# Kernel optimization log

Measured on AMD Instinct MI355X. Metric: run time of the kernel, lower is better.

Reference implementation:

```python
import jax, jax.numpy as jnp
import numpy as np

B, L, D = 4, 2048, 1024
H, DH = 16, 64
W = 128            # window_len
CS, R = 32, 1      # chunk_size, chunk_rank
CACHE = 2048
NCC = CACHE // CS * R   # compressed cache vectors (64)
NCB = L // CS * R       # compressed block vectors (64)
NC = NCC + NCB          # total compressed vectors (128)
NQ = L // CS            # query chunks (64)
T = L // W              # query tiles (16)
NEG = jnp.float32(-1e30)


def _ln(x, g, b, eps=1e-5):
    m = x.mean(-1, keepdims=True)
    v = ((x - m) ** 2).mean(-1, keepdims=True)
    return (x - m) * jax.lax.rsqrt(v + eps) * g + b


def _scores(x, Wd, bd):
    # dconv_1 + per-chunk softmax over chunk_size positions
    b = x.shape[0]; nc = x.shape[1] // CS
    s = (x @ Wd + bd).reshape(b, nc, CS, H, R)
    s = jnp.transpose(s, (0, 3, 1, 4, 2))          # b,H,nc,R,CS
    return jax.nn.softmax(s.astype(jnp.float32), axis=-1).astype(x.dtype)


def _compress(x, sc):
    b = x.shape[0]; nc = x.shape[1] // CS
    xv = jnp.transpose(x.reshape(b, nc, CS, H, DH), (0, 3, 1, 2, 4))  # b,H,nc,CS,DH
    return (sc @ xv).reshape(b, H, nc * R, DH)


def _heads(x):
    b, l, _ = x.shape
    return jnp.transpose(x.reshape(b, l, H, DH), (0, 2, 1, 3))


def _rel_shift(x):
    # Transformer-XL style relative shift, chunk variant (zeros enter from padding)
    b = x.shape[0]; nc = x.shape[-1]
    x5 = jnp.transpose(x.reshape(b, H, NQ, CS, nc), (0, 1, 3, 2, 4))  # b,H,CS,NQ,nc
    xp = jnp.pad(x5, ((0, 0), (0, 0), (0, 0), (0, 0), (0, R))).reshape(b, H, CS, NQ * (nc + R))
    idx = NQ * R + jnp.arange(NQ)[:, None] * nc + jnp.arange(nc)[None, :]
    out = jnp.take(xp, idx.reshape(-1), axis=-1).reshape(b, H, CS, NQ, nc)
    return jnp.transpose(out, (0, 1, 3, 2, 4)).reshape(b, H, L, nc)


def _forward(h, h_cache, key_pe, pos_win, Wq, Wk, Wv, Wo, Wd, bd, Wr, br, Wrc, brc,
             r_r_bias, r_w_bias, g_dproj, b_dproj, g_win, b_win, mask):
    b = h.shape[0]
    q = _heads(h @ Wq) / np.float32(np.sqrt(DH))       # b,H,L,DH (pre-scaled)

    # --- compressed cache keys/values ---
    hcc = _compress(h_cache, _scores(h_cache, Wd, bd))           # b,H,NCC,DH
    hcm = jnp.transpose(hcc, (0, 2, 1, 3)).reshape(b, -1, D)
    k_cache = _heads(_ln(hcm @ Wk, g_dproj, b_dproj))
    v_cache = _heads(_ln(hcm @ Wv, g_dproj, b_dproj))

    # --- sliding window keys/values (last W of cache + current block) ---
    k_bp = h @ Wk
    v_bp = h @ Wv
    hw = h_cache[:, -W:]
    k_win = _ln(jnp.concatenate([hw @ Wk, k_bp], 1), g_win, b_win)   # b, W+L, D
    v_win = _ln(jnp.concatenate([hw @ Wv, v_bp], 1), g_win, b_win)

    # --- compressed current-block keys/values ---
    sc = _scores(h, Wd, bd)
    k_bpc = _heads(_ln(jnp.transpose(_compress(k_bp, sc), (0, 2, 1, 3)).reshape(b, -1, D), g_dproj, b_dproj))
    v_bpc = _heads(_ln(jnp.transpose(_compress(v_bp, sc), (0, 2, 1, 3)).reshape(b, -1, D), g_dproj, b_dproj))
    k_comp = jnp.concatenate([k_cache, k_bpc], 2)     # b,H,NC,DH
    v_comp = jnp.concatenate([v_cache, v_bpc], 2)

    # --- windowed attention (tiled, as_strided equivalent via gather) ---
    ti = jnp.arange(T)[:, None] * W + jnp.arange(2 * W)[None, :]     # (T, 2W)
    k_t = jnp.transpose(k_win[:, ti].reshape(b, T, 2 * W, H, DH), (0, 3, 1, 2, 4))  # b,H,T,2W,DH
    v_t = jnp.transpose(v_win[:, ti].reshape(b, T, 2 * W, H, DH), (0, 3, 1, 2, 4))
    q_t = q.reshape(b, H, T, W, DH)
    aw = jnp.einsum('bhtqd,bhtkd->bhtqk', q_t + r_w_bias, k_t)       # b,H,T,W,2W
    # diagonal extraction: row q keeps cols q+1 .. q+W (the W causal window keys)
    dcol = jnp.arange(W)[:, None] + 1 + jnp.arange(W)[None, :]       # (W, W)
    aw = jnp.take_along_axis(aw, dcol[None, None, None], axis=-1).reshape(b, H, L, W)
    pos_t = (pos_win @ Wr + br).reshape(W, H, DH)
    aw = aw + jnp.einsum('bhld,whd->bhlw', q + r_r_bias, pos_t)

    # --- compressed (chunk) attention ---
    ac = jnp.einsum('bhld,bhcd->bhlc', q, k_comp)
    pos_c = (key_pe @ Wrc + brc).reshape(NC, H, DH)
    ac = ac + _rel_shift(jnp.einsum('bhld,chd->bhlc', q, pos_c))
    ac = jnp.where(mask, NEG, ac.reshape(b, H, NQ, CS, NC)).reshape(b, H, L, NC)

    # --- joint softmax over [compressed | window] ---
    full = jax.nn.softmax(jnp.concatenate([ac, aw], -1).astype(jnp.float32), -1).astype(h.dtype)
    ac, aw = full[..., :NC], full[..., NC:]

    # --- put_tiles: scatter window probs back to tiled 2W layout (inverse of diag extract) ---
    awt = aw.reshape(b, H, T, W, W)
    awp = jnp.pad(awt, ((0, 0), (0, 0), (0, 0), (0, 0), (1, W)))     # last dim 1+2W, zeros outside band
    col = jnp.clip(jnp.arange(2 * W)[None, :] - jnp.arange(W)[:, None], 0, 2 * W)
    aw_t = jnp.take_along_axis(awp, col[None, None, None], axis=-1)  # b,H,T,W,2W

    out = jnp.einsum('bhlc,bhcd->bhld', ac, v_comp) + \
          jnp.einsum('bhtqk,bhtkd->bhtqd', aw_t, v_t).reshape(b, H, L, DH)
    out = jnp.transpose(out, (0, 2, 1, 3)).reshape(b, L, D)
    return out @ Wo


def setup_inputs() -> dict:
    key = jax.random.key(0)
    ks = jax.random.split(key, 16)
    p = lambda i, shape: jax.random.normal(ks[i], shape, jnp.float32) * 0.02
    inp = dict(
        h=jax.random.normal(ks[0], (B, L, D), jnp.float32),
        h_cache=jax.random.normal(ks[1], (B, CACHE, D), jnp.float32),
        key_pe=jax.random.normal(ks[2], (NC, D), jnp.float32),
        pos_embed_window=jax.random.normal(ks[3], (W, D), jnp.float32),
        Wq=p(4, (D, D)), Wk=p(5, (D, D)), Wv=p(6, (D, D)), Wo=p(7, (D, D)),
        Wd=p(8, (D, H * R)), bd=jnp.zeros((H * R,), jnp.float32),
        Wr=p(9, (D, D)), br=jnp.zeros((D,), jnp.float32),
        Wrc=p(10, (D, D)), brc=jnp.zeros((D,), jnp.float32),
        r_r_bias=p(11, (1, H, 1, DH)), r_w_bias=p(12, (1, H, 1, 1, DH)),
        g_dproj=jnp.ones((D,), jnp.float32), b_dproj=jnp.zeros((D,), jnp.float32),
        g_win=jnp.ones((D,), jnp.float32), b_win=jnp.zeros((D,), jnp.float32),
    )
    # causal mask over compressed vectors: bp chunk c visible to query chunk j only if c < j
    jq = jnp.arange(NQ)[:, None]
    cc = jnp.arange(NCB // R)[None, :]
    mbp = jnp.repeat(cc >= jq, R, axis=1)                         # (NQ, NCB)
    mask = jnp.concatenate([jnp.zeros((NQ, NCC), bool), mbp], axis=1)
    inp['chunked_attn_mask'] = mask[None, None, :, None, :]       # (1,1,NQ,1,NC)
    return inp


def reference(h, h_cache, key_pe, pos_embed_window, Wq, Wk, Wv, Wo, Wd, bd, Wr, br,
              Wrc, brc, r_r_bias, r_w_bias, g_dproj, b_dproj, g_win, b_win,
              chunked_attn_mask):
    return _forward(h, h_cache, key_pe, pos_embed_window, Wq, Wk, Wv, Wo, Wd, bd,
                    Wr, br, Wrc, brc, r_r_bias, r_w_bias, g_dproj, b_dproj,
                    g_win, b_win, chunked_attn_mask)
```

## Files before the change

kernel.cpp:

```cpp
#include <hip/hip_runtime.h>


typedef unsigned short u16;
typedef __attribute__((ext_vector_type(8))) short short8;
typedef __attribute__((ext_vector_type(4))) float f32x4;

#define NEGINF -1e30f

__device__ __forceinline__ float bf2f(u16 u) {
    union { unsigned int i; float f; } v; v.i = ((unsigned int)u) << 16; return v.f;
}
__device__ __forceinline__ u16 f2bf(float f) {
    union { float fl; unsigned int i; } v; v.fl = f;
    unsigned int x = v.i;
    return (u16)((x + 0x7fffu + ((x >> 16) & 1u)) >> 16);
}
__device__ __forceinline__ short8 ldg8(const u16* p) { return *(const short8*)p; }

__device__ __forceinline__ void async16(const u16* g, u16* l) {
    __builtin_amdgcn_global_load_lds(
        (const __attribute__((address_space(1))) unsigned int*)g,
        (__attribute__((address_space(3))) unsigned int*)l, 16, 0, 0);
}

__global__ __launch_bounds__(256) void cast_all(
    const float* __restrict__ h, const float* __restrict__ hc,
    const float* __restrict__ pos_w, const float* __restrict__ key_pe,
    const float* __restrict__ Wd,
    u16* __restrict__ hB, u16* __restrict__ hcwB,
    u16* __restrict__ pwB, u16* __restrict__ kpeB, u16* __restrict__ WdB)
{
    const int bx = blockIdx.x, tid = threadIdx.x;
    if (bx < 8192) {
        int i = bx * 256 + tid;
        float4 v = ((const float4*)h)[i];
        u16* o = hB + (long)i * 4;
        o[0] = f2bf(v.x); o[1] = f2bf(v.y); o[2] = f2bf(v.z); o[3] = f2bf(v.w);
    } else if (bx < 8704) {
        int i = (bx - 8192) * 256 + tid;
        int flat = i * 4;
        int b = flat >> 17, r = (flat >> 10) & 127, c = flat & 1023;
        float4 v = *(const float4*)(hc + ((long)b * 2048 + 1920 + r) * 1024 + c);
        u16* o = hcwB + (long)flat;
        o[0] = f2bf(v.x); o[1] = f2bf(v.y); o[2] = f2bf(v.z); o[3] = f2bf(v.w);
    } else if (bx < 8832) {
        int i = (bx - 8704) * 256 + tid;
        float4 v = ((const float4*)pos_w)[i];
        u16* o = pwB + (long)i * 4;
        o[0] = f2bf(v.x); o[1] = f2bf(v.y); o[2] = f2bf(v.z); o[3] = f2bf(v.w);
    } else if (bx < 8960) {
        int i = (bx - 8832) * 256 + tid;
        float4 v = ((const float4*)key_pe)[i];
        u16* o = kpeB + (long)i * 4;
        o[0] = f2bf(v.x); o[1] = f2bf(v.y); o[2] = f2bf(v.z); o[3] = f2bf(v.w);
    } else {
        int e = (bx - 8960) * 256 + tid;
        if (e < 16384) WdB[(e & 15) * 1024 + (e >> 4)] = f2bf(Wd[e]);
    }
}

__global__ __launch_bounds__(256) void cast_transpose6(
    const float* __restrict__ W0, const float* __restrict__ W1,
    const float* __restrict__ W2, const float* __restrict__ W3,
    const float* __restrict__ W4, const float* __restrict__ W5,
    u16* __restrict__ D0, u16* __restrict__ D1, u16* __restrict__ D2,
    u16* __restrict__ D3, u16* __restrict__ D4, u16* __restrict__ D5)
{
    const int z = blockIdx.z;
    const float* W = (z == 0) ? W0 : (z == 1) ? W1 : (z == 2) ? W2
                   : (z == 3) ? W3 : (z == 4) ? W4 : W5;
    u16* WT = (z == 0) ? D0 : (z == 1) ? D1 : (z == 2) ? D2
            : (z == 3) ? D3 : (z == 4) ? D4 : D5;

    __shared__ float t[32][33];
    const int bx = blockIdx.x, by = blockIdx.y;
    const int tx = threadIdx.x & 31, ty = threadIdx.x >> 5;
    #pragma unroll
    for (int p = 0; p < 4; ++p) {
        int k = by * 32 + ty + p * 8;
        t[ty + p * 8][tx] = W[(long)k * 1024 + bx * 32 + tx];
    }
    __syncthreads();
    #pragma unroll
    for (int p = 0; p < 4; ++p) {
        int n = ty + p * 8;
        WT[((long)(bx * 32 + n)) * 1024 + by * 32 + tx] = f2bf(t[tx][n]);
    }
}

#define GEMM_P3_BODY(EPILOGUE)                                                  \
    const int tid = threadIdx.x;                                                \
    const int bm = blockIdx.x, bn = blockIdx.y;                                 \
    const int K = 1024, NT = 32;                                                \
    __shared__ __align__(16) u16 As[3 * 128 * 32];                              \
    __shared__ __align__(16) u16 Bs[3 * 128 * 32];                              \
    const int lane = tid & 63, wv = tid >> 6;                                   \
    const int l15 = lane & 15, quad = lane >> 4;                                \
    const int wm = (wv & 1) * 64, wn = (wv >> 1) * 64;                          \
    f32x4 acc[4][4];                                                            \
    _Pragma("unroll")                                                           \
    for (int i = 0; i < 4; ++i)                                                 \
        _Pragma("unroll")                                                       \
        for (int j = 0; j < 4; ++j) acc[i][j] = (f32x4){0.f, 0.f, 0.f, 0.f};    \
    const int srow = wv * 32 + (lane >> 2);                                     \
    const int scol = (lane & 3) * 8;                                            \
    const u16* a_src  = A  + (long)(bm * 128 + srow) * K + scol;                \
    const u16* a_src2 = a_src + (long)16 * K;                                   \
    const u16* b_src  = Bt + (long)(bn * 128 + srow) * K + scol;                \
    const u16* b_src2 = b_src + (long)16 * K;                                   \
    const int lofs0 = (wv * 32) * 32;                                           \
    const int lofs1 = (wv * 32 + 16) * 32;                                      \
    auto stage = [&](int t, int cur) {                                          \
        const int k0 = t * 32;                                                  \
        async16(a_src  + k0, &As[cur * 4096 + lofs0]);                          \
        async16(a_src2 + k0, &As[cur * 4096 + lofs1]);                          \
        async16(b_src  + k0, &Bs[cur * 4096 + lofs0]);                          \
        async16(b_src2 + k0, &Bs[cur * 4096 + lofs1]);                          \
    };                                                                          \
    stage(0, 0); stage(1, 1);                                                   \
    int cur = 0;                                                                \
    for (int t = 0; t < NT; ++t) {                                              \
        if (t == NT - 1)                                                        \
            asm volatile("s_waitcnt vmcnt(0) lgkmcnt(0)\ns_barrier" ::: "memory"); \
        else                                                                    \
            asm volatile("s_waitcnt vmcnt(4) lgkmcnt(0)\ns_barrier" ::: "memory"); \
        int nxt = cur + 2; if (nxt >= 3) nxt -= 3;                              \
        if (t + 2 < NT) stage(t + 2, nxt);                                      \
        const u16* as = &As[cur * 4096];                                        \
        const u16* bs = &Bs[cur * 4096];                                        \
        short8 af[4], bfr[4];                                                   \
        _Pragma("unroll")                                                       \
        for (int i = 0; i < 4; ++i)                                             \
            af[i] = *(const short8*)&as[(wm + i * 16 + l15) * 32 + quad * 8];   \
        _Pragma("unroll")                                                       \
        for (int j = 0; j < 4; ++j)                                             \
            bfr[j] = *(const short8*)&bs[(wn + j * 16 + l15) * 32 + quad * 8];  \
        _Pragma("unroll")                                                       \
        for (int i = 0; i < 4; ++i)                                             \
            _Pragma("unroll")                                                   \
            for (int j = 0; j < 4; ++j)                                         \
                acc[i][j] = __builtin_amdgcn_mfma_f32_16x16x32_bf16(af[i], bfr[j], acc[i][j], 0, 0, 0); \
        cur = (cur + 1 == 3) ? 0 : cur + 1;                                     \
    }                                                                           \
    EPILOGUE

__global__ __launch_bounds__(256) void gemm_qkv3(
    const u16* __restrict__ A, const u16* __restrict__ Bt,
    u16* __restrict__ q_ws, u16* __restrict__ kbp, u16* __restrict__ vbp)
{
    GEMM_P3_BODY({
        const int mat = bn >> 3;
        _Pragma("unroll")
        for (int i = 0; i < 4; ++i) {
            _Pragma("unroll")
            for (int j = 0; j < 4; ++j) {
                int col = (bn & 7) * 128 + wn + j * 16 + l15;
                _Pragma("unroll")
                for (int r = 0; r < 4; ++r) {
                    int row = bm * 128 + wm + i * 16 + quad * 4 + r;
                    float v = acc[i][j][r];
                    long idx = (long)row * 1024 + col;
                    if (mat == 0)      q_ws[idx] = f2bf(v * 0.125f);
                    else if (mat == 1) kbp[idx] = f2bf(v);
                    else               vbp[idx] = f2bf(v);
                }
            }
        }
    })
}

__global__ __launch_bounds__(256) void gemm_out3(
    const u16* __restrict__ A, const u16* __restrict__ Bt,
    float* __restrict__ Cf)
{
    GEMM_P3_BODY({
        _Pragma("unroll")
        for (int i = 0; i < 4; ++i) {
            _Pragma("unroll")
            for (int j = 0; j < 4; ++j) {
                int col = bn * 128 + wn + j * 16 + l15;
                _Pragma("unroll")
                for (int r = 0; r < 4; ++r) {
                    int row = bm * 128 + wm + i * 16 + quad * 4 + r;
                    Cf[(long)row * 1024 + col] = acc[i][j][r];
                }
            }
        }
    })
}

struct GJob {
    const u16* A; long ab;
    const u16* Bt;
    float* Cf; u16* Cb; long cb;
    const float* bias; float scale;
};

__device__ __forceinline__ void gemm_core128(
    const GJob& j, int bz, int bm, int bn, int N, int K)
{
    const int tid = threadIdx.x;
    const u16* A = j.A + (long)bz * j.ab;
    const long coff = (long)bz * j.cb;

    __shared__ __align__(16) u16 As[128 * 32];
    __shared__ __align__(16) u16 Bs[128 * 32];

    const int lane = tid & 63, wv = tid >> 6;
    const int l15 = lane & 15, quad = lane >> 4;
    const int wm = (wv & 1) * 64, wn = (wv >> 1) * 64;

    f32x4 acc[4][4];
    #pragma unroll
    for (int i = 0; i < 4; ++i)
        #pragma unroll
        for (int jx = 0; jx < 4; ++jx) acc[i][jx] = (f32x4){0.f, 0.f, 0.f, 0.f};

    const int srow = wv * 32 + (lane >> 2);
    const int scol = (lane & 3) * 8;
    const u16* a_src  = A    + (long)(bm * 128 + srow) * K + scol;
    const u16* a_src2 = a_src + (long)16 * K;
    const u16* b_src  = j.Bt + (long)(bn * 128 + srow) * K + scol;
    const u16* b_src2 = b_src + (long)16 * K;
    u16* lA0 = &As[(wv * 32) * 32];
    u16* lA1 = &As[(wv * 32 + 16) * 32];
    u16* lB0 = &Bs[(wv * 32) * 32];
    u16* lB1 = &Bs[(wv * 32 + 16) * 32];

    for (int k0 = 0; k0 < K; k0 += 32) {
        async16(a_src, lA0); async16(a_src2, lA1);
        async16(b_src, lB0); async16(b_src2, lB1);
        a_src += 32; a_src2 += 32; b_src += 32; b_src2 += 32;
        __syncthreads();
        short8 af[4], bfr[4];
        #pragma unroll
        for (int i = 0; i < 4; ++i)
            af[i] = *(const short8*)&As[(wm + i * 16 + l15) * 32 + quad * 8];
        #pragma unroll
        for (int jx = 0; jx < 4; ++jx)
            bfr[jx] = *(const short8*)&Bs[(wn + jx * 16 + l15) * 32 + quad * 8];
        #pragma unroll
        for (int i = 0; i < 4; ++i)
            #pragma unroll
            for (int jx = 0; jx < 4; ++jx)
                acc[i][jx] = __builtin_amdgcn_mfma_f32_16x16x32_bf16(af[i], bfr[jx], acc[i][jx], 0, 0, 0);
        __syncthreads();
    }

    #pragma unroll
    for (int i = 0; i < 4; ++i) {
        #pragma unroll
        for (int jx = 0; jx < 4; ++jx) {
            int col = bn * 128 + wn + jx * 16 + l15;
            float bsv = j.bias ? j.bias[col] : 0.f;
            #pragma unroll
            for (int r = 0; r < 4; ++r) {
                int row = bm * 128 + wm + i * 16 + quad * 4 + r;
                float v = acc[i][jx][r] * j.scale + bsv;
                long idx = coff + (long)row * N + col;
                if (j.Cf) j.Cf[idx] = v;
                if (j.Cb) j.Cb[idx] = f2bf(v);
            }
        }
    }
}

__global__ __launch_bounds__(256) void gemm_dual(GJob j0, GJob j1, int nz0, int N, int K)
{
    const bool first = ((int)blockIdx.z < nz0);
    const int bz = first ? blockIdx.z : blockIdx.z - nz0;
    if (first) gemm_core128(j0, bz, blockIdx.x, blockIdx.y, N, K);
    else       gemm_core128(j1, bz, blockIdx.x, blockIdx.y, N, K);
}

__global__ __launch_bounds__(256) void gemm_multi4(GJob j0, GJob j1, GJob j2, GJob j3,
                                                   int n0, int n1, int n2, int N, int K)
{
    const int z = blockIdx.z;
    if (z < n0)                gemm_core128(j0, z, blockIdx.x, blockIdx.y, N, K);
    else if (z < n0 + n1)      gemm_core128(j1, z - n0, blockIdx.x, blockIdx.y, N, K);
    else if (z < n0 + n1 + n2) gemm_core128(j2, z - n0 - n1, blockIdx.x, blockIdx.y, N, K);
    else                       gemm_core128(j3, z - n0 - n1 - n2, blockIdx.x, blockIdx.y, N, K);
}

__global__ __launch_bounds__(256) void scores_compress2(
    const float* __restrict__ hc, const u16* __restrict__ hBp,
    const u16* __restrict__ WdB, const float* __restrict__ bd,
    u16* __restrict__ hcm, float* __restrict__ sc_blk)
{
    const int c = blockIdx.x, b = blockIdx.y;
    const bool zc = (blockIdx.z == 0);
    const int tid = threadIdx.x;
    const int lane = tid & 63, wv = tid >> 6;
    const int l15 = lane & 15, quad = lane >> 4;

    __shared__ __align__(16) u16 srcs[32][1032];
    __shared__ float sred[4][32][16];
    __shared__ float s_sm[32][16];

    if (zc) {
        const float* sb = hc + (long)b * 2048 * 1024 + (long)c * 32 * 1024;
        for (int e = tid; e < 8192; e += 256) {
            int flat = e * 4;
            int row = flat >> 10, col = flat & 1023;
            float4 v = *(const float4*)(sb + (long)row * 1024 + col);
            u16* dp = &srcs[row][col];
            dp[0] = f2bf(v.x); dp[1] = f2bf(v.y); dp[2] = f2bf(v.z); dp[3] = f2bf(v.w);
        }
    } else {
        const u16* sb = hBp + (long)b * 2048 * 1024 + (long)c * 32 * 1024;
        for (int e = tid; e < 4096; e += 256) {
            int flat = e * 8;
            int row = flat >> 10, col = flat & 1023;
            *(short8*)&srcs[row][col] = ldg8(sb + (long)row * 1024 + col);
        }
    }
    __syncthreads();

    {
        f32x4 acc0 = {0.f,0.f,0.f,0.f}, acc1 = {0.f,0.f,0.f,0.f};
        const int kq = wv * 256;
        #pragma unroll
        for (int kc = 0; kc < 8; ++kc) {
            int off = kq + kc * 32 + quad * 8;
            short8 bf_ = ldg8(WdB + (long)l15 * 1024 + off);
            short8 a0 = *(const short8*)&srcs[l15][off];
            short8 a1 = *(const short8*)&srcs[16 + l15][off];
            acc0 = __builtin_amdgcn_mfma_f32_16x16x32_bf16(a0, bf_, acc0, 0, 0, 0);
            acc1 = __builtin_amdgcn_mfma_f32_16x16x32_bf16(a1, bf_, acc1, 0, 0, 0);
        }
        #pragma unroll
        for (int r = 0; r < 4; ++r) {
            sred[wv][quad * 4 + r][l15]      = acc0[r];
            sred[wv][16 + quad * 4 + r][l15] = acc1[r];
        }
    }
    __syncthreads();
    for (int idx = tid; idx < 512; idx += 256) {
        int i = idx >> 4, hd = idx & 15;
        s_sm[i][hd] = bd[hd] + sred[0][i][hd] + sred[1][i][hd]
                            + sred[2][i][hd] + sred[3][i][hd];
    }
    __syncthreads();

    if (tid < 16) {
        int hd = tid;
        float m = NEGINF;
        for (int i = 0; i < 32; ++i) m = fmaxf(m, s_sm[i][hd]);
        float s = 0.f;
        for (int i = 0; i < 32; ++i) s += __expf(s_sm[i][hd] - m);
        float inv = 1.f / s;
        for (int i = 0; i < 32; ++i) s_sm[i][hd] = __expf(s_sm[i][hd] - m) * inv;
    }
    __syncthreads();

    if (!zc) {
        for (int idx = tid; idx < 512; idx += 256) {
            int hd = idx >> 5, i = idx & 31;
            sc_blk[(long)b * (16*64*32) + ((long)hd * 64 + c) * 32 + i] = s_sm[i][hd];
        }
    } else {
        #pragma unroll
        for (int p = 0; p < 4; ++p) {
            int j = tid + p * 256;
            int hd = j >> 6;
            float acc = 0.f;
            for (int i = 0; i < 32; ++i) acc += s_sm[i][hd] * bf2f(srcs[i][j]);
            hcm[(long)b * (64*1024) + (long)c * 1024 + j] = f2bf(acc);
        }
    }
}

__global__ __launch_bounds__(256) void compress_kv_ln(
    const u16* __restrict__ kbp, const u16* __restrict__ vbp,
    const float* __restrict__ sc,
    const float* __restrict__ g, const float* __restrict__ be,
    u16* __restrict__ k_comp, u16* __restrict__ vcT)
{
    const int c = blockIdx.x, b = blockIdx.y;
    const int tid = threadIdx.x;
    const int lane = tid & 63, wv = tid >> 6;

    __shared__ float scw[16][32];
    __shared__ float red[4][4];

    for (int idx = tid; idx < 512; idx += 256) {
        int hd = idx >> 5, i = idx & 31;
        scw[hd][i] = sc[((long)(b * 16 + hd) * 64 + c) * 32 + i];
    }
    __syncthreads();

    const int j0 = tid * 4;
    const int hd = j0 >> 6;
    float xk[4] = {0.f,0.f,0.f,0.f}, xv[4] = {0.f,0.f,0.f,0.f};
    const u16* kb = kbp + ((long)b * 2048 + c * 32) * 1024 + j0;
    const u16* vb = vbp + ((long)b * 2048 + c * 32) * 1024 + j0;
    for (int i = 0; i < 32; ++i) {
        float w = scw[hd][i];
        uint2 kr = *(const uint2*)(kb + (long)i * 1024);
        uint2 vr = *(const uint2*)(vb + (long)i * 1024);
        const u16* kp = (const u16*)&kr;
        const u16* vp = (const u16*)&vr;
        #pragma unroll
        for (int p = 0; p < 4; ++p) {
            xk[p] += w * bf2f(kp[p]);
            xv[p] += w * bf2f(vp[p]);
        }
    }
    float sk = 0.f, qk = 0.f, sv = 0.f, qv = 0.f;
    #pragma unroll
    for (int p = 0; p < 4; ++p) { sk += xk[p]; qk += xk[p]*xk[p]; sv += xv[p]; qv += xv[p]*xv[p]; }
    for (int off = 32; off; off >>= 1) {
        sk += __shfl_xor(sk, off); qk += __shfl_xor(qk, off);
        sv += __shfl_xor(sv, off); qv += __shfl_xor(qv, off);
    }
    if (lane == 0) { red[0][wv] = sk; red[1][wv] = qk; red[2][wv] = sv; red[3][wv] = qv; }
    __syncthreads();
    sk = red[0][0] + red[0][1] + red[0][2] + red[0][3];
    qk = red[1][0] + red[1][1] + red[1][2] + red[1][3];
    sv = red[2][0] + red[2][1] + red[2][2] + red[2][3];
    qv = red[3][0] + red[3][1] + red[3][2] + red[3][3];
    const float inv_n = 1.f / 1024.f;
    float mk = sk * inv_n, mv = sv * inv_n;
    float ik = rsqrtf(fmaxf(qk * inv_n - mk * mk, 0.f) + 1e-5f);
    float iv = rsqrtf(fmaxf(qv * inv_n - mv * mv, 0.f) + 1e-5f);
    float4 g4 = *(const float4*)(g + j0);
    float4 b4 = *(const float4*)(be + j0);
    float gg[4] = {g4.x, g4.y, g4.z, g4.w};
    float bb[4] = {b4.x, b4.y, b4.z, b4.w};
    u16 ko[4];
    #pragma unroll
    for (int p = 0; p < 4; ++p) ko[p] = f2bf((xk[p] - mk) * ik * gg[p] + bb[p]);
    *(uint2*)&k_comp[((long)b * 128 + 64 + c) * 1024 + j0] = *(const uint2*)ko;
    #pragma unroll
    for (int p = 0; p < 4; ++p)
        vcT[((long)b * 1024 + j0 + p) * 128 + 64 + c] = f2bf((xv[p] - mv) * iv * gg[p] + bb[p]);
}

__global__ __launch_bounds__(256) void ln_rows_kv(
    const float* __restrict__ kc, const float* __restrict__ vc,
    const float* __restrict__ g, const float* __restrict__ be,
    u16* __restrict__ k_comp, u16* __restrict__ vcT)
{
    const int gr = blockIdx.x;
    const int b = gr >> 6, r = gr & 63;
    const float* pk = kc + ((long)b * 64 + r) * 1024;
    const float* pv = vc + ((long)b * 64 + r) * 1024;
    const int tid = threadIdx.x;
    const int lane = tid & 63, wv = tid >> 6;

    __shared__ float red[4][4];
    float xk[4], xv[4];
    float smk = 0.f, sqk = 0.f, smv = 0.f, sqv = 0.f;
    #pragma unroll
    for (int p = 0; p < 4; ++p) {
        xk[p] = pk[tid + p * 256];
        xv[p] = pv[tid + p * 256];
        smk += xk[p]; sqk += xk[p] * xk[p];
        smv += xv[p]; sqv += xv[p] * xv[p];
    }
    for (int off = 32; off; off >>= 1) {
        smk += __shfl_xor(smk, off); sqk += __shfl_xor(sqk, off);
        smv += __shfl_xor(smv, off); sqv += __shfl_xor(sqv, off);
    }
    if (lane == 0) { red[0][wv] = smk; red[1][wv] = sqk; red[2][wv] = smv; red[3][wv] = sqv; }
    __syncthreads();
    smk = red[0][0] + red[0][1] + red[0][2] + red[0][3];
    sqk = red[1][0] + red[1][1] + red[1][2] + red[1][3];
    smv = red[2][0] + red[2][1] + red[2][2] + red[2][3];
    sqv = red[3][0] + red[3][1] + red[3][2] + red[3][3];
    const float inv_n = 1.f / 1024.f;
    float mk = smk * inv_n, mv = smv * inv_n;
    float ik = rsqrtf(fmaxf(sqk * inv_n - mk * mk, 0.f) + 1e-5f);
    float iv = rsqrtf(fmaxf(sqv * inv_n - mv * mv, 0.f) + 1e-5f);
    #pragma unroll
    for (int p = 0; p < 4; ++p) {
        int j = tid + p * 256;
        k_comp[((long)b * 128 + r) * 1024 + j] = f2bf((xk[p] - mk) * ik * g[j] + be[j]);
        vcT[((long)b * 1024 + j) * 128 + r]    = f2bf((xv[p] - mv) * iv * g[j] + be[j]);
    }
}

__global__ __launch_bounds__(256) void row_stats_all(
    const float* __restrict__ kcw, const float* __restrict__ vcw,
    const u16* __restrict__ kbp, const u16* __restrict__ vbp,
    float2* __restrict__ st_k, float2* __restrict__ st_v)
{
    const int gr = blockIdx.x;
    const int tid = threadIdx.x;
    const int lane = tid & 63, wv = tid >> 6;

    float sm1 = 0.f, sq1 = 0.f, sm2 = 0.f, sq2 = 0.f;
    long dst;
    if (gr < 512) {
        const int b = gr >> 7, r = gr & 127;
        const float* p1 = kcw + ((long)b * 128 + r) * 1024;
        const float* p2 = vcw + ((long)b * 128 + r) * 1024;
        #pragma unroll
        for (int p = 0; p < 4; ++p) {
            float x = p1[tid + p * 256];
            float y = p2[tid + p * 256];
            sm1 += x; sq1 += x * x;
            sm2 += y; sq2 += y * y;
        }
        dst = (long)b * 2176 + r;
    } else {
        const int g2 = gr - 512;
        const int b = g2 >> 11, r = g2 & 2047;
        const u16* p1 = kbp + ((long)b * 2048 + r) * 1024 + tid * 4;
        const u16* p2 = vbp + ((long)b * 2048 + r) * 1024 + tid * 4;
        uint2 v1 = *(const uint2*)p1;
        uint2 v2 = *(const uint2*)p2;
        const u16* a1 = (const u16*)&v1;
        const u16* a2 = (const u16*)&v2;
        #pragma unroll
        for (int p = 0; p < 4; ++p) {
            float x = bf2f(a1[p]);
            float y = bf2f(a2[p]);
            sm1 += x; sq1 += x * x;
            sm2 += y; sq2 += y * y;
        }
        dst = (long)b * 2176 + 128 + r;
    }

    __shared__ float red[4][4];
    for (int off = 32; off; off >>= 1) {
        sm1 += __shfl_xor(sm1, off); sq1 += __shfl_xor(sq1, off);
        sm2 += __shfl_xor(sm2, off); sq2 += __shfl_xor(sq2, off);
    }
    if (lane == 0) { red[0][wv] = sm1; red[1][wv] = sq1; red[2][wv] = sm2; red[3][wv] = sq2; }
    __syncthreads();
    if (tid == 0) {
        sm1 = red[0][0] + red[0][1] + red[0][2] + red[0][3];
        sq1 = red[1][0] + red[1][1] + red[1][2] + red[1][3];
        sm2 = red[2][0] + red[2][1] + red[2][2] + red[2][3];
        sq2 = red[3][0] + red[3][1] + red[3][2] + red[3][3];
        float m1 = sm1 * (1.f / 1024.f);
        float i1 = rsqrtf(fmaxf(sq1 * (1.f / 1024.f) - m1 * m1, 0.f) + 1e-5f);
        float m2 = sm2 * (1.f / 1024.f);
        float i2 = rsqrtf(fmaxf(sq2 * (1.f / 1024.f) - m2 * m2, 0.f) + 1e-5f);
        st_k[dst] = make_float2(m1, i1);
        st_v[dst] = make_float2(m2, i2);
    }
}

__global__ __launch_bounds__(256) void win_apply(
    const float* __restrict__ kcw, const float* __restrict__ vcw,
    const u16* __restrict__ kbp, const u16* __restrict__ vbp,
    const float2* __restrict__ st_kw, const float2* __restrict__ st_vw,
    const float* __restrict__ g_w, const float* __restrict__ b_w,
    u16* __restrict__ kwin, u16* __restrict__ vwinT)
{
    const int tt = blockIdx.x, dc = blockIdx.y, b = blockIdx.z;
    const int t0 = tt * 64, d0 = dc * 64;
    const int tid = threadIdx.x;

    __shared__ u16 vt[64][74];

    const int r = tid >> 2;
    const int dsub = (tid & 3) * 16;
    const int t = t0 + r;
    float2 sk = st_kw[(long)b * 2176 + t];
    float2 sv = st_vw[(long)b * 2176 + t];
    const float* ksf = kcw + ((long)b * 128 + t) * 1024;
    const float* vsf = vcw + ((long)b * 128 + t) * 1024;
    const u16*   ksb = kbp + ((long)b * 2048 + t - 128) * 1024;
    const u16*   vsb = vbp + ((long)b * 2048 + t - 128) * 1024;
    #pragma unroll
    for (int j = 0; j < 16; j += 4) {
        int d = d0 + dsub + j;
        float4 kv, vv;
        if (t < 128) {
            kv = *(const float4*)(ksf + d);
            vv = *(const float4*)(vsf + d);
        } else {
            uint2 kr = *(const uint2*)(ksb + d);
            uint2 vr = *(const uint2*)(vsb + d);
            const u16* kp = (const u16*)&kr;
            const u16* vp = (const u16*)&vr;
            kv = make_float4(bf2f(kp[0]), bf2f(kp[1]), bf2f(kp[2]), bf2f(kp[3]));
            vv = make_float4(bf2f(vp[0]), bf2f(vp[1]), bf2f(vp[2]), bf2f(vp[3]));
        }
        float4 g4 = *(const float4*)(g_w + d);
        float4 b4 = *(const float4*)(b_w + d);
        u16 ko[4];
        ko[0] = f2bf((kv.x - sk.x) * sk.y * g4.x + b4.x);
        ko[1] = f2bf((kv.y - sk.x) * sk.y * g4.y + b4.y);
        ko[2] = f2bf((kv.z - sk.x) * sk.y * g4.z + b4.z);
        ko[3] = f2bf((kv.w - sk.x) * sk.y * g4.w + b4.w);
        *(uint2*)&kwin[((long)b * 2176 + t) * 1024 + d] = *(const uint2*)ko;
        vt[r][dsub + j + 0] = f2bf((vv.x - sv.x) * sv.y * g4.x + b4.x);
        vt[r][dsub + j + 1] = f2bf((vv.y - sv.x) * sv.y * g4.y + b4.y);
        vt[r][dsub + j + 2] = f2bf((vv.z - sv.x) * sv.y * g4.z + b4.z);
        vt[r][dsub + j + 3] = f2bf((vv.w - sv.x) * sv.y * g4.w + b4.w);
    }
    __syncthreads();
    #pragma unroll
    for (int pass = 0; pass < 16; ++pass) {
        int dd = (tid >> 6) + pass * 4;
        int rr = tid & 63;
        int crow = t0 + rr;
        if (crow >= 1)
            vwinT[((long)b * 1024 + d0 + dd) * 2176 + crow - 1] = vt[rr][dd];
    }
}

__global__ __launch_bounds__(256, 4) void attention(
    const u16* __restrict__ qb,
    const u16* __restrict__ kcb,
    const u16* __restrict__ vcT,
    const u16* __restrict__ kwb,
    const u16* __restrict__ vwT,
    const u16* __restrict__ pcb,
    const u16* __restrict__ ptb,
    const float* __restrict__ r_w,
    const float* __restrict__ r_r,
    u16* __restrict__ attn_o)
{
    const int qc = blockIdx.x, h = blockIdx.y, b = blockIdx.z;
    const int l0 = qc * 32;
    const int tid = threadIdx.x;
    const int lane = tid & 63, wv = tid >> 6;
    const int l15 = lane & 15, quad = lane >> 4;

    __shared__ __align__(16) float L[32 * 260];
    __shared__ __align__(16) u16 qa[32][72];
    u16* Lu = (u16*)L;

    {
        const int r = tid >> 3, d0 = (tid & 7) * 8;
        short8 qv = ldg8(qb + ((long)(b * 2048 + l0 + r)) * 1024 + h * 64 + d0);
        *(short8*)&qa[r][d0] = qv;
    }
    __syncthreads();

    __builtin_amdgcn_s_setprio(1);
    #pragma unroll
    for (int ti = 0; ti < 2; ++ti) {
        int n0 = (wv * 2 + ti) * 16;
        int ci = n0 + l15;
        f32x4 a0 = {0.f,0.f,0.f,0.f}, a1 = {0.f,0.f,0.f,0.f};
        if (n0 < 64 + qc) {
            int p = 64 + ci - qc; if (p > 127) p = 127;
            #pragma unroll
            for (int kc = 0; kc < 2; ++kc) {
                int k0 = kc * 32;
                short8 bk = ldg8(kcb + ((long)(b * 128 + ci)) * 1024 + h * 64 + k0 + quad * 8);
                short8 bp = ldg8(pcb + (long)p * 1024 + h * 64 + k0 + quad * 8);
                short8 fa0 = *(const short8*)&qa[l15][k0 + quad * 8];
                short8 fa1 = *(const short8*)&qa[16 + l15][k0 + quad * 8];
                a0 = __builtin_amdgcn_mfma_f32_16x16x32_bf16(fa0, bk, a0, 0, 0, 0);
                a0 = __builtin_amdgcn_mfma_f32_16x16x32_bf16(fa0, bp, a0, 0, 0, 0);
                a1 = __builtin_amdgcn_mfma_f32_16x16x32_bf16(fa1, bk, a1, 0, 0, 0);
                a1 = __builtin_amdgcn_mfma_f32_16x16x32_bf16(fa1, bp, a1, 0, 0, 0);
            }
        }
        bool msk = (ci >= 64 + qc);
        #pragma unroll
        for (int r = 0; r < 4; ++r) {
            L[(quad * 4 + r) * 260 + ci]      = msk ? NEGINF : a0[r];
            L[(16 + quad * 4 + r) * 260 + ci] = msk ? NEGINF : a1[r];
        }
    }

    {
        short8 qf[2][2];
        #pragma unroll
        for (int kc = 0; kc < 2; ++kc) {
            const int off = kc * 32 + quad * 8;
            const float* bp_ = r_r + h * 64 + off;
            float4 b0 = *(const float4*)bp_;
            float4 b1 = *(const float4*)(bp_ + 4);
            float bb[8] = {b0.x,b0.y,b0.z,b0.w,b1.x,b1.y,b1.z,b1.w};
            #pragma unroll
            for (int hf = 0; hf < 2; ++hf) {
                short8 qv = *(const short8*)&qa[hf * 16 + l15][off];
                short8 f;
                #pragma unroll
                for (int j = 0; j < 8; ++j) f[j] = (short)f2bf(bf2f((u16)qv[j]) + bb[j]);
                qf[kc][hf] = f;
            }
        }
        #pragma unroll
        for (int ti = 0; ti < 2; ++ti) {
            int w0 = (wv * 2 + ti) * 16;
            int w = w0 + l15;
            f32x4 a0 = {0.f,0.f,0.f,0.f}, a1 = {0.f,0.f,0.f,0.f};
            #pragma unroll
            for (int kc = 0; kc < 2; ++kc) {
                int k0 = kc * 32;
                short8 bp = ldg8(ptb + (long)w * 1024 + h * 64 + k0 + quad * 8);
                a0 = __builtin_amdgcn_mfma_f32_16x16x32_bf16(qf[kc][0], bp, a0, 0, 0, 0);
                a1 = __builtin_amdgcn_mfma_f32_16x16x32_bf16(qf[kc][1], bp, a1, 0, 0, 0);
            }
            #pragma unroll
            for (int r = 0; r < 4; ++r) {
                L[(quad * 4 + r) * 260 + 128 + w]      = a0[r];
                L[(16 + quad * 4 + r) * 260 + 128 + w] = a1[r];
            }
        }
    }

    f32x4 s1a[3], s1b[3];
    int nts[3]; int nw = 0;
    {
        short8 qf[2][2];
        #pragma unroll
        for (int kc = 0; kc < 2; ++kc) {
            const int off = kc * 32 + quad * 8;
            const float* bp_ = r_w + h * 64 + off;
            float4 b0 = *(const float4*)bp_;
            float4 b1 = *(const float4*)(bp_ + 4);
            float bb[8] = {b0.x,b0.y,b0.z,b0.w,b1.x,b1.y,b1.z,b1.w};
            #pragma unroll
            for (int hf = 0; hf < 2; ++hf) {
                short8 qv = *(const short8*)&qa[hf * 16 + l15][off];
                short8 f;
                #pragma unroll
                for (int j = 0; j < 8; ++j) f[j] = (short)f2bf(bf2f((u16)qv[j]) + bb[j]);
                qf[kc][hf] = f;
            }
        }
        for (int nt = wv; nt < 10; nt += 4) {
            int t = nt * 16 + l15;
            int row = l0 + 1 + t; if (row > 2175) row = 2175;
            f32x4 a0 = {0.f,0.f,0.f,0.f}, a1 = {0.f,0.f,0.f,0.f};
            #pragma unroll
            for (int kc = 0; kc < 2; ++kc) {
                int k0 = kc * 32;
                short8 bk = ldg8(kwb + ((long)(b * 2176 + row)) * 1024 + h * 64 + k0 + quad * 8);
                a0 = __builtin_amdgcn_mfma_f32_16x16x32_bf16(qf[kc][0], bk, a0, 0, 0, 0);
                a1 = __builtin_amdgcn_mfma_f32_16x16x32_bf16(qf[kc][1], bk, a1, 0, 0, 0);
            }
            s1a[nw] = a0; s1b[nw] = a1; nts[nw] = nt; ++nw;
        }
    }
    __builtin_amdgcn_s_setprio(0);
    __syncthreads();
    for (int i = 0; i < nw; ++i) {
        int t = nts[i] * 16 + l15;
        #pragma unroll
        for (int r = 0; r < 4; ++r) {
            int r0 = quad * 4 + r;
            int w0 = t - r0;
            if (w0 >= 0 && w0 < 128) L[r0 * 260 + 128 + w0] += s1a[i][r];
            int r1 = 16 + quad * 4 + r;
            int w1 = t - r1;
            if (w1 >= 0 && w1 < 128) L[r1 * 260 + 128 + w1] += s1b[i][r];
        }
    }
    __syncthreads();

    const int n0d = wv * 16;
    short8 bvv[9];
    {
        const u16* vc = vcT + ((long)(b * 1024 + h * 64 + n0d + l15)) * 128 + quad * 8;
        #pragma unroll
        for (int kc = 0; kc < 4; ++kc) bvv[kc] = ldg8(vc + kc * 32);
        const u16* vw = vwT + ((long)(b * 1024 + h * 64 + n0d + l15)) * 2176 + l0 + quad * 8;
        #pragma unroll
        for (int kc = 0; kc < 5; ++kc) bvv[4 + kc] = ldg8(vw + kc * 32);
    }

    #pragma unroll
    for (int rr = 0; rr < 8; ++rr) {
        const int r = wv * 8 + rr;
        float4 v = *(const float4*)&L[r * 260 + lane * 4];
        float m = fmaxf(fmaxf(v.x, v.y), fmaxf(v.z, v.w));
        for (int off = 32; off; off >>= 1) m = fmaxf(m, __shfl_xor(m, off));
        float e0 = __expf(v.x - m), e1 = __expf(v.y - m);
        float e2 = __expf(v.z - m), e3 = __expf(v.w - m);
        float s = (e0 + e1) + (e2 + e3);
        for (int off = 32; off; off >>= 1) s += __shfl_xor(s, off);
        float inv = 1.f / s;
        e0 *= inv; e1 *= inv; e2 *= inv; e3 *= inv;
        u16* rowP = Lu + (long)r * 520;
        if (lane < 32) {
            u16 pk[4] = {f2bf(e0), f2bf(e1), f2bf(e2), f2bf(e3)};
            *(uint2*)&rowP[lane * 4] = *(const uint2*)pk;
        } else {
            const int l = lane - 32;
            const int t = 4 * l + r;
            u16* p = rowP + 160 + t;
            p[0] = f2bf(e0); p[1] = f2bf(e1); p[2] = f2bf(e2); p[3] = f2bf(e3);
            const int tz = (l < r) ? l : 128 + l;
            rowP[160 + tz] = 0;
        }
    }
    __syncthreads();

    __builtin_amdgcn_s_setprio(1);
    f32x4 o0 = {0.f,0.f,0.f,0.f}, o1 = {0.f,0.f,0.f,0.f};
    #pragma unroll
    for (int kc = 0; kc < 4; ++kc) {
        int k0 = kc * 32;
        short8 av0 = *(const short8*)(Lu + (long)l15 * 520 + k0 + quad * 8);
        short8 av1 = *(const short8*)(Lu + (long)(16 + l15) * 520 + k0 + quad * 8);
        o0 = __builtin_amdgcn_mfma_f32_16x16x32_bf16(av0, bvv[kc], o0, 0, 0, 0);
        o1 = __builtin_amdgcn_mfma_f32_16x16x32_bf16(av1, bvv[kc], o1, 0, 0, 0);
    }
    #pragma unroll
    for (int kc = 0; kc < 5; ++kc) {
        int k0 = kc * 32;
        short8 av0 = *(const short8*)(Lu + (long)l15 * 520 + 160 + k0 + quad * 8);
        short8 av1 = *(const short8*)(Lu + (long)(16 + l15) * 520 + 160 + k0 + quad * 8);
        o0 = __builtin_amdgcn_mfma_f32_16x16x32_bf16(av0, bvv[4 + kc], o0, 0, 0, 0);
        o1 = __builtin_amdgcn_mfma_f32_16x16x32_bf16(av1, bvv[4 + kc], o1, 0, 0, 0);
    }
    __builtin_amdgcn_s_setprio(0);
    #pragma unroll
    for (int r = 0; r < 4; ++r) {
        int r0 = quad * 4 + r, r1 = 16 + quad * 4 + r;
        attn_o[((long)(b * 2048 + l0 + r0)) * 1024 + h * 64 + n0d + l15] = f2bf(o0[r]);
        attn_o[((long)(b * 2048 + l0 + r1)) * 1024 + h * 64 + n0d + l15] = f2bf(o1[r]);
    }
}

extern "C" void kernel_launch(void* const* d_in, const int* in_sizes, int n_in,
                              void* d_out, int out_size, void* d_ws, size_t ws_size,
                              hipStream_t stream)
{
    (void)in_sizes; (void)n_in; (void)out_size; (void)ws_size;

    const float* h       = (const float*)d_in[0];
    const float* h_cache = (const float*)d_in[1];
    const float* key_pe  = (const float*)d_in[2];
    const float* pos_w   = (const float*)d_in[3];
    const float* Wq      = (const float*)d_in[4];
    const float* Wk      = (const float*)d_in[5];
    const float* Wv      = (const float*)d_in[6];
    const float* Wo      = (const float*)d_in[7];
    const float* Wd      = (const float*)d_in[8];
    const float* bd      = (const float*)d_in[9];
    const float* Wr      = (const float*)d_in[10];
    const float* br      = (const float*)d_in[11];
    const float* Wrc     = (const float*)d_in[12];
    const float* brc     = (const float*)d_in[13];
    const float* r_r     = (const float*)d_in[14];
    const float* r_w     = (const float*)d_in[15];
    const float* g_d     = (const float*)d_in[16];
    const float* b_d     = (const float*)d_in[17];
    const float* g_w     = (const float*)d_in[18];
    const float* b_w     = (const float*)d_in[19];

    char* ws = (char*)d_ws;
    size_t off = 0;
    auto alloc = [&](size_t bytes) -> void* {
        void* p = ws + off; off += (bytes + 255) & ~(size_t)255; return p;
    };
    u16* hB     = (u16*)alloc((size_t)8192 * 1024 * 2);
    u16* hcwB   = (u16*)alloc((size_t)4 * 128 * 1024 * 2);
    u16* WqkvT  = (u16*)alloc((size_t)3 * 1024 * 1024 * 2);
    u16* WoT    = (u16*)alloc((size_t)1024 * 1024 * 2);
    u16* WrT    = (u16*)alloc((size_t)1024 * 1024 * 2);
    u16* WrcT   = (u16*)alloc((size_t)1024 * 1024 * 2);
    u16* pwB    = (u16*)alloc((size_t)128 * 1024 * 2);
    u16* kpeB   = (u16*)alloc((size_t)128 * 1024 * 2);
    u16* WdB    = (u16*)alloc((size_t)16 * 1024 * 2);
    u16*   q_ws   = (u16*)alloc((size_t)8192 * 1024 * 2);
    u16*   kbp    = (u16*)alloc((size_t)8192 * 1024 * 2);
    u16*   vbp    = (u16*)alloc((size_t)8192 * 1024 * 2);
    u16*   attn_o = (u16*)alloc((size_t)8192 * 1024 * 2);
    float* kcw    = (float*)alloc((size_t)4 * 128 * 1024 * 4);
    float* vcw    = (float*)alloc((size_t)4 * 128 * 1024 * 4);
    u16*   hcm    = (u16*)alloc((size_t)4 * 64 * 1024 * 2);
    float* kc_raw = (float*)alloc((size_t)4 * 64 * 1024 * 4);
    float* vc_raw = (float*)alloc((size_t)4 * 64 * 1024 * 4);
    float* sc_blk = (float*)alloc((size_t)4 * 16 * 64 * 32 * 4);
    u16*   k_comp = (u16*)alloc((size_t)4 * 128 * 1024 * 2);
    u16*   vcT    = (u16*)alloc((size_t)4 * 1024 * 128 * 2);
    float2* st_kw = (float2*)alloc((size_t)4 * 2176 * 8);
    float2* st_vw = (float2*)alloc((size_t)4 * 2176 * 8);
    u16*   pos_tb = (u16*)alloc((size_t)128 * 1024 * 2);
    u16*   pos_cb = (u16*)alloc((size_t)128 * 1024 * 2);
    u16*   kwin   = (u16*)alloc((size_t)4 * 2176 * 1024 * 2);
    u16*   vwinT  = (u16*)alloc((size_t)4 * 1024 * 2176 * 2 + 256);

    const u16* WkT = WqkvT + (size_t)1024 * 1024;
    const u16* WvT = WqkvT + (size_t)2 * 1024 * 1024;

    const dim3 blk(256);

    cast_all<<<dim3(9024), blk, 0, stream>>>(h, h_cache, pos_w, key_pe, Wd,
                                             hB, hcwB, pwB, kpeB, WdB);
    cast_transpose6<<<dim3(32,32,6), blk, 0, stream>>>(
        Wq, Wk, Wv, Wo, Wr, Wrc,
        WqkvT, WqkvT + (size_t)1024*1024, WqkvT + (size_t)2*1024*1024,
        WoT, WrT, WrcT);

    {
        GJob jk = { hcwB, (long)128*1024, WkT, kcw, nullptr, (long)128*1024, nullptr, 1.f };
        GJob jv = { hcwB, (long)128*1024, WvT, vcw, nullptr, (long)128*1024, nullptr, 1.f };
        GJob jt = { pwB,  0, WrT,  nullptr, pos_tb, 0, br,  1.f };
        GJob jc = { kpeB, 0, WrcT, nullptr, pos_cb, 0, brc, 1.f };
        gemm_multi4<<<dim3(1,8,10), blk, 0, stream>>>(jk, jv, jt, jc, 4, 4, 1, 1024, 1024);
    }

    gemm_qkv3<<<dim3(64,24,1), blk, 0, stream>>>(hB, WqkvT, q_ws, kbp, vbp);

    scores_compress2<<<dim3(64,4,2), blk, 0, stream>>>(h_cache, hB, WdB, bd, hcm, sc_blk);

    {
        GJob jk = { hcm, 0, WkT, kc_raw, nullptr, 0, nullptr, 1.f };
        GJob jv = { hcm, 0, WvT, vc_raw, nullptr, 0, nullptr, 1.f };
        gemm_dual<<<dim3(2,8,2), blk, 0, stream>>>(jk, jv, 1, 1024, 1024);
    }

    compress_kv_ln<<<dim3(64,4), blk, 0, stream>>>(kbp, vbp, sc_blk, g_d, b_d, k_comp, vcT);
    ln_rows_kv<<<dim3(256), blk, 0, stream>>>(kc_raw, vc_raw, g_d, b_d, k_comp, vcT);

    row_stats_all<<<dim3(8704), blk, 0, stream>>>(kcw, vcw, kbp, vbp, st_kw, st_vw);
    win_apply<<<dim3(34,16,4), blk, 0, stream>>>(kcw, vcw, kbp, vbp, st_kw, st_vw, g_w, b_w, kwin, vwinT);

    attention<<<dim3(64,16,4), blk, 0, stream>>>(q_ws, k_comp, vcT, kwin, vwinT,
                                                 pos_cb, pos_tb, r_w, r_r, attn_o);
    gemm_out3<<<dim3(64,8,1), blk, 0, stream>>>(attn_o, WoT, (float*)d_out);
}
```

Measured before the change: 508.5 us.

## Replace QKV GEMM with 256x256-tile 512-thread kernel and LDS-staged epilogue

Replaces the 128x128-tile, triple-buffered QKV projection GEMM with a 256x256-tile kernel using 512 threads, double-buffered async global-to-LDS loads, and 8x4 MFMA accumulators per wave. Half the waves load A and half load B. Results are staged through LDS so the output is written as coalesced 16-byte stores instead of scattered 2-byte stores. The larger tile raises arithmetic intensity, but the grid shrinks to 384 blocks, which can hurt occupancy and load balance across CUs. Register pressure also goes up with 128 accumulator floats per thread.

```diff
diff --git a/kernel.cpp b/kernel.cpp
--- a/kernel.cpp
+++ b/kernel.cpp
@@ -85,6 +85,105 @@
     for (int p = 0; p < 4; ++p) {
         int n = ty + p * 8;
         WT[((long)(bx * 32 + n)) * 1024 + by * 32 + tx] = f2bf(t[tx][n]);
+    }
+}
+
+__global__ __launch_bounds__(512) void gemm_qkv_big(
+    const u16* __restrict__ A, const u16* __restrict__ Bt,
+    u16* __restrict__ q_ws, u16* __restrict__ kbp, u16* __restrict__ vbp)
+{
+    const int tid = threadIdx.x;
+    const int bm = blockIdx.x, bn = blockIdx.y;
+    const int K = 1024, NT = 32;
+
+    __shared__ __align__(16) u16 smem[65536 / 2];
+    u16* const As = smem;
+    u16* const Bs = smem + 16384;
+
+    const int lane = tid & 63, wv = tid >> 6;
+    const int l15 = lane & 15, quad = lane >> 4;
+    const int wm = (wv >> 2) * 128, wn = (wv & 3) * 64;
+
+    f32x4 acc[8][4];
+    #pragma unroll
+    for (int i = 0; i < 8; ++i)
+        #pragma unroll
+        for (int j = 0; j < 4; ++j) acc[i][j] = (f32x4){0.f, 0.f, 0.f, 0.f};
+
+    const int r_in = lane >> 2, col8 = (lane & 3) * 8;
+    const bool isA = (wv < 4);
+    const int crow0 = (isA ? wv : wv - 4) * 64;
+    const u16* gb = isA ? (A + (long)(bm * 256 + crow0 + r_in) * K)
+                        : (Bt + (long)(bn * 256 + crow0 + r_in) * K);
+    const u16* s0 = gb + col8;
+    const u16* s1 = s0 + (long)16 * K;
+    const u16* s2 = s0 + (long)32 * K;
+    const u16* s3 = s0 + (long)48 * K;
+    u16* const lb = (isA ? As : Bs) + crow0 * 32;
+
+    auto stage = [&](int buf) {
+        u16* d = lb + buf * 8192;
+        async16(s0, d);
+        async16(s1, d + 512);
+        async16(s2, d + 1024);
+        async16(s3, d + 1536);
+        s0 += 32; s1 += 32; s2 += 32; s3 += 32;
+    };
+
+    stage(0);
+    for (int t = 0; t < NT; ++t) {
+        __builtin_amdgcn_s_barrier();
+        if (t + 1 < NT) {
+            stage((t + 1) & 1);
+            asm volatile("s_waitcnt vmcnt(4) lgkmcnt(0)\ns_barrier" ::: "memory");
+        } else {
+            asm volatile("s_waitcnt vmcnt(0) lgkmcnt(0)\ns_barrier" ::: "memory");
+        }
+        const u16* as = As + (t & 1) * 8192;
+        const u16* bs = Bs + (t & 1) * 8192;
+        short8 af[8], bfr[4];
+        #pragma unroll
+        for (int i = 0; i < 8; ++i)
+            af[i] = *(const short8*)&as[(wm + i * 16 + l15) * 32 + quad * 8];
+        #pragma unroll
+        for (int j = 0; j < 4; ++j)
+            bfr[j] = *(const short8*)&bs[(wn + j * 16 + l15) * 32 + quad * 8];
+        #pragma unroll
+        for (int i = 0; i < 8; ++i)
+            #pragma unroll
+            for (int j = 0; j < 4; ++j)
+                acc[i][j] = __builtin_amdgcn_mfma_f32_16x16x32_bf16(af[i], bfr[j], acc[i][j], 0, 0, 0);
+    }
+
+    const int mat = bn >> 2;
+    u16* const outp = (mat == 0) ? q_ws : (mat == 1) ? kbp : vbp;
+    const float scl = (mat == 0) ? 0.125f : 1.f;
+    const int colbase = (bn & 3) * 256;
+    #pragma unroll
+    for (int hh = 0; hh < 2; ++hh) {
+        __syncthreads();
+        if ((wv >> 2) == hh) {
+            #pragma unroll
+            for (int i = 0; i < 8; ++i) {
+                #pragma unroll
+                for (int j = 0; j < 4; ++j) {
+                    const int row = i * 16 + quad * 4;
+                    const int col = wn + j * 16 + l15;
+                    smem[(row + 0) * 256 + col] = f2bf(acc[i][j][0] * scl);
+                    smem[(row + 1) * 256 + col] = f2bf(acc[i][j][1] * scl);
+                    smem[(row + 2) * 256 + col] = f2bf(acc[i][j][2] * scl);
+                    smem[(row + 3) * 256 + col] = f2bf(acc[i][j][3] * scl);
+                }
+            }
+        }
+        __syncthreads();
+        #pragma unroll
+        for (int k = 0; k < 8; ++k) {
+            const int seg = tid + k * 512;
+            const int row = seg >> 5, c16 = seg & 31;
+            short8 v = *(const short8*)&smem[row * 256 + c16 * 8];
+            *(short8*)(outp + (long)(bm * 256 + hh * 128 + row) * 1024 + colbase + c16 * 8) = v;
+        }
     }
 }
 
@@ -144,31 +243,6 @@
     }                                                                           \
     EPILOGUE
 
-__global__ __launch_bounds__(256) void gemm_qkv3(
-    const u16* __restrict__ A, const u16* __restrict__ Bt,
-    u16* __restrict__ q_ws, u16* __restrict__ kbp, u16* __restrict__ vbp)
-{
-    GEMM_P3_BODY({
-        const int mat = bn >> 3;
-        _Pragma("unroll")
-        for (int i = 0; i < 4; ++i) {
-            _Pragma("unroll")
-            for (int j = 0; j < 4; ++j) {
-                int col = (bn & 7) * 128 + wn + j * 16 + l15;
-                _Pragma("unroll")
-                for (int r = 0; r < 4; ++r) {
-                    int row = bm * 128 + wm + i * 16 + quad * 4 + r;
-                    float v = acc[i][j][r];
-                    long idx = (long)row * 1024 + col;
-                    if (mat == 0)      q_ws[idx] = f2bf(v * 0.125f);
-                    else if (mat == 1) kbp[idx] = f2bf(v);
-                    else               vbp[idx] = f2bf(v);
-                }
-            }
-        }
-    })
-}
-
 __global__ __launch_bounds__(256) void gemm_out3(
     const u16* __restrict__ A, const u16* __restrict__ Bt,
     float* __restrict__ Cf)
@@ -896,7 +970,7 @@
         gemm_multi4<<<dim3(1,8,10), blk, 0, stream>>>(jk, jv, jt, jc, 4, 4, 1, 1024, 1024);
     }
 
-    gemm_qkv3<<<dim3(64,24,1), blk, 0, stream>>>(hB, WqkvT, q_ws, kbp, vbp);
+    gemm_qkv_big<<<dim3(32,12), dim3(512), 0, stream>>>(hB, WqkvT, q_ws, kbp, vbp);
 
     scores_compress2<<<dim3(64,4,2), blk, 0, stream>>>(h_cache, hB, WdB, bd, hcm, sc_blk);
 
```

New measurement: 467.3 us. -8.1%, faster.
